# Kernel tuning notes

Measured on AMD Instinct MI355X. Metric: run time of the kernel, lower is better.

The kernel has to match this reference:

```python
import jax, jax.numpy as jnp
import numpy as np
import math

B, L, D = 2, 2048, 1024
H, KV, HD = 16, 4, 64          # num_heads, num_kv_heads, head_dim
GROUPS = H // KV
ROPE_BASE = 10000.0


def _alibi_slopes(n_heads):
    def pow2(n):
        start = 2.0 ** (-(2.0 ** (-(math.log2(n) - 3))))
        return [start * (start ** i) for i in range(n)]
    if math.log2(n_heads).is_integer():
        return pow2(n_heads)
    c = 2 ** math.floor(math.log2(n_heads))
    return pow2(c) + _alibi_slopes(2 * c)[0::2][: n_heads - c]


def _rope_cos_sin(seq_len, dim, dtype):
    inv_freq = 1.0 / (ROPE_BASE ** (jnp.arange(0, dim, 2, dtype=jnp.float32) / dim))
    t = jnp.arange(seq_len, dtype=jnp.float32)
    freqs = t[:, None] * inv_freq[None, :]          # [L, dim/2]
    emb = jnp.concatenate([freqs, freqs], axis=-1)  # [L, dim]
    return jnp.cos(emb).astype(dtype), jnp.sin(emb).astype(dtype)


def _rotate_half(x):
    x1, x2 = x[..., : x.shape[-1] // 2], x[..., x.shape[-1] // 2 :]
    return jnp.concatenate([-x2, x1], axis=-1)


def setup_inputs() -> dict:
    key = jax.random.key(0)
    ks = jax.random.split(key, 5)
    s = 0.02
    return {
        "x": jax.random.normal(ks[0], (B, L, D), jnp.float32),
        "Wq": jax.random.normal(ks[1], (D, H * HD), jnp.float32) * s,
        "Wk": jax.random.normal(ks[2], (D, KV * HD), jnp.float32) * s,
        "Wv": jax.random.normal(ks[3], (D, KV * HD), jnp.float32) * s,
        "Wo": jax.random.normal(ks[4], (H * HD, D), jnp.float32) * s,
    }


def reference(x, Wq, Wk, Wv, Wo):
    b, l, _ = x.shape
    q = (x @ Wq).reshape(b, l, H, HD).transpose(0, 2, 1, 3)   # [B,H,L,hd]
    k = (x @ Wk).reshape(b, l, KV, HD).transpose(0, 2, 1, 3)  # [B,KV,L,hd]
    v = (x @ Wv).reshape(b, l, KV, HD).transpose(0, 2, 1, 3)
    # MQA broadcast: repeat_interleave over head dim
    k = jnp.repeat(k, GROUPS, axis=1)  # [B,H,L,hd]
    v = jnp.repeat(v, GROUPS, axis=1)

    cos, sin = _rope_cos_sin(l, HD, x.dtype)  # [L,hd]
    q = q * cos + _rotate_half(q) * sin
    k = k * cos + _rotate_half(k) * sin

    attn = jnp.einsum("bhqd,bhkd->bhqk", q, k) / math.sqrt(HD)
    # ALiBi bias: (j - i) * slope_h
    pos = jnp.arange(l)
    rel = (pos[None, :] - pos[:, None]).astype(x.dtype)        # [L,L]
    slopes = jnp.asarray(_alibi_slopes(H), dtype=x.dtype)      # [H]
    attn = attn + slopes[None, :, None, None] * rel[None, None, :, :]

    attn = jax.nn.softmax(attn, axis=-1)
    out = jnp.einsum("bhqk,bhkd->bhqd", attn, v)               # [B,H,L,hd]
    out = out.transpose(0, 2, 1, 3).reshape(b, l, H * HD)
    return out @ Wo
```

## Files before the change

kernel.cpp:

```cpp
#include <hip/hip_runtime.h>
#include <math.h>

typedef unsigned short u16;
typedef unsigned int u32;
typedef __attribute__((ext_vector_type(8))) short short8;
typedef __attribute__((ext_vector_type(4))) short short4v;
typedef __attribute__((ext_vector_type(4))) float floatx4;
typedef __attribute__((ext_vector_type(2))) unsigned int uint2v;

#define HN 16
#define KVN 4
#define HDN 64
#define BN_ 2
#define LN 2048
#define DN 1024

__device__ __forceinline__ u16 f2bf(float f) {
    u32 u = __float_as_uint(f);
    u32 r = (u + 0x7fffu + ((u >> 16) & 1u)) >> 16;
    return (u16)r;
}

__device__ __forceinline__ u32 pack2bf(float f0, float f1) {
    u32 u0 = __float_as_uint(f0);
    u32 u1 = __float_as_uint(f1);
    u0 += 0x7fffu + ((u0 >> 16) & 1u);
    u1 += 0x7fffu + ((u1 >> 16) & 1u);
    return __builtin_amdgcn_perm(u1, u0, 0x07060302u);
}

__device__ __forceinline__ void gl16(const u16* g, u16* l) {
    __builtin_amdgcn_global_load_lds(
        (const __attribute__((address_space(1))) u32*)g,
        (__attribute__((address_space(3))) u32*)l, 16, 0, 0);
}

__device__ __forceinline__ void do_transpose(const float* __restrict__ W, u16* __restrict__ WT,
                                             int R, int C, int bx, int by, int tid,
                                             float (*t)[33]) {
    int tx = tid & 31, ty = tid >> 5;
    int c0 = bx * 32, r0 = by * 32;
#pragma unroll
    for (int i = 0; i < 4; i++) {
        int r = r0 + ty + i * 8;
        t[ty + i * 8][tx] = W[(size_t)r * C + c0 + tx];
    }
    __syncthreads();
#pragma unroll
    for (int i = 0; i < 4; i++) {
        int c = c0 + ty + i * 8;
        WT[(size_t)c * R + r0 + tx] = f2bf(t[tx][ty + i * 8]);
    }
}

__global__ __launch_bounds__(256) void prep_kernel(const float* __restrict__ x,
                                                   const float* __restrict__ Wq,
                                                   const float* __restrict__ Wk,
                                                   const float* __restrict__ Wv,
                                                   const float* __restrict__ Wo,
                                                   u16* __restrict__ xb,
                                                   u16* __restrict__ WT,
                                                   u16* __restrict__ WoT) {
    __shared__ float t[32][33];
    int blk = blockIdx.x, tid = threadIdx.x;
    if (blk < 4096) {
        int i = blk * 256 + tid;
        floatx4 v = ((const floatx4*)x)[i];
        short4v o;
        o[0] = (short)f2bf(v[0]);
        o[1] = (short)f2bf(v[1]);
        o[2] = (short)f2bf(v[2]);
        o[3] = (short)f2bf(v[3]);
        ((short4v*)xb)[i] = o;
    } else if (blk < 5120) {
        int z = blk - 4096;
        do_transpose(Wq, WT, 1024, 1024, z & 31, z >> 5, tid, t);
    } else if (blk < 5376) {
        int z = blk - 5120;
        do_transpose(Wk, WT + 1024 * 1024, 1024, 256, z & 7, z >> 3, tid, t);
    } else if (blk < 5632) {
        int z = blk - 5376;
        do_transpose(Wv, WT + 1280 * 1024, 1024, 256, z & 7, z >> 3, tid, t);
    } else {
        int z = blk - 5632;
        do_transpose(Wo, WoT, 1024, 1024, z & 31, z >> 5, tid, t);
    }
}

__global__ __launch_bounds__(256) void gemm_qkv_rope(const u16* __restrict__ A,
                                                     const u16* __restrict__ BT,
                                                     u16* __restrict__ Qb,
                                                     u16* __restrict__ Kb,
                                                     u16* __restrict__ Vt) {
    __shared__ u16 sm[12288];
    const int K = 1024;
    int tid = threadIdx.x;
    int w = tid >> 6, l = tid & 63, quad = l >> 4, l16 = l & 15;
    int wm = w * 32;
    floatx4 acc[2][4];
#pragma unroll
    for (int i = 0; i < 2; i++)
#pragma unroll
        for (int j = 0; j < 4; j++) acc[i][j] = (floatx4){0.f, 0.f, 0.f, 0.f};
    const u16* ag0 = A + (size_t)(blockIdx.y * 128 + (tid >> 2)) * K + (tid & 3) * 8;
    const u16* ag1 = ag0 + (size_t)64 * K;
    const u16* bg = BT + (size_t)(blockIdx.x * 64 + (tid >> 2)) * K + (tid & 3) * 8;
    int lbase = tid * 8;
    gl16(ag0, &sm[lbase]);
    gl16(ag1, &sm[2048 + lbase]);
    gl16(bg, &sm[4096 + lbase]);
    for (int it = 0; it < 32; it++) {
        __syncthreads();
        int cur = it & 1;
        if (it + 1 < 32) {
            int nb = (cur ^ 1) * 6144;
            ag0 += 32; ag1 += 32; bg += 32;
            gl16(ag0, &sm[nb + lbase]);
            gl16(ag1, &sm[nb + 2048 + lbase]);
            gl16(bg, &sm[nb + 4096 + lbase]);
        }
        const u16* sa = &sm[cur * 6144];
        const u16* sb = sa + 4096;
        short8 af[2], bfr[4];
#pragma unroll
        for (int mt = 0; mt < 2; mt++) af[mt] = *(const short8*)&sa[(wm + mt * 16 + l16) * 32 + quad * 8];
#pragma unroll
        for (int nt = 0; nt < 4; nt++) bfr[nt] = *(const short8*)&sb[(nt * 16 + l16) * 32 + quad * 8];
#pragma unroll
        for (int mt = 0; mt < 2; mt++)
#pragma unroll
            for (int nt = 0; nt < 4; nt++)
                acc[mt][nt] = __builtin_amdgcn_mfma_f32_16x16x32_bf16(af[mt], bfr[nt], acc[mt][nt], 0, 0, 0);
    }
    int bx = blockIdx.x;
    int row0 = blockIdx.y * 128 + wm;
    const float L2R32 = 0.4152410118609203f;
    if (bx < 20) {
        int isK = (bx >= 16);
        int head = isK ? (bx - 16) : bx;
        u16* dst = isK ? Kb : Qb;
        size_t bstride = (size_t)(isK ? KVN : HN) * LN * HDN;
        float invf[2];
#pragma unroll
        for (int ntp = 0; ntp < 2; ntp++) invf[ntp] = exp2f(-(float)(ntp * 16 + l16) * L2R32);
        dst += (size_t)head * LN * HDN;
#pragma unroll
        for (int mt = 0; mt < 2; mt++)
#pragma unroll
            for (int r = 0; r < 4; r++) {
                int row = row0 + mt * 16 + quad * 4 + r;
                int b = row >> 11;
                int lpos = row & 2047;
                float lf = (float)lpos;
#pragma unroll
                for (int ntp = 0; ntp < 2; ntp++) {
                    float th = lf * invf[ntp];
                    float s, c;
                    __sincosf(th, &s, &c);
                    float x1 = acc[mt][ntp][r], x2 = acc[mt][ntp + 2][r];
                    size_t base = (size_t)b * bstride + ((size_t)lpos) * HDN + ntp * 16 + l16;
                    dst[base] = f2bf(x1 * c - x2 * s);
                    dst[base + 32] = f2bf(x2 * c + x1 * s);
                }
            }
    } else {
        int kv = bx - 20;
#pragma unroll
        for (int mt = 0; mt < 2; mt++)
#pragma unroll
            for (int r = 0; r < 4; r++) {
                int row = row0 + mt * 16 + quad * 4 + r;
                int b = row >> 11;
                int lpos = row & 2047;
#pragma unroll
                for (int nt = 0; nt < 4; nt++) {
                    int d = nt * 16 + l16;
                    Vt[(((size_t)b * KVN + kv) * HDN + d) * LN + lpos] = f2bf(acc[mt][nt][r]);
                }
            }
    }
}

__global__ __launch_bounds__(256) void gemm_out(const u16* __restrict__ A,
                                                const u16* __restrict__ BT,
                                                float* __restrict__ C) {
    __shared__ u16 sm[12288];
    const int K = 1024, N = 1024;
    int tid = threadIdx.x;
    int w = tid >> 6, l = tid & 63, quad = l >> 4, l16 = l & 15;
    int wm = w * 32;
    floatx4 acc[2][4];
#pragma unroll
    for (int i = 0; i < 2; i++)
#pragma unroll
        for (int j = 0; j < 4; j++) acc[i][j] = (floatx4){0.f, 0.f, 0.f, 0.f};
    const u16* ag0 = A + (size_t)(blockIdx.y * 128 + (tid >> 2)) * K + (tid & 3) * 8;
    const u16* ag1 = ag0 + (size_t)64 * K;
    const u16* bg = BT + (size_t)(blockIdx.x * 64 + (tid >> 2)) * K + (tid & 3) * 8;
    int lbase = tid * 8;
    gl16(ag0, &sm[lbase]);
    gl16(ag1, &sm[2048 + lbase]);
    gl16(bg, &sm[4096 + lbase]);
    for (int it = 0; it < 32; it++) {
        __syncthreads();
        int cur = it & 1;
        if (it + 1 < 32) {
            int nb = (cur ^ 1) * 6144;
            ag0 += 32; ag1 += 32; bg += 32;
            gl16(ag0, &sm[nb + lbase]);
            gl16(ag1, &sm[nb + 2048 + lbase]);
            gl16(bg, &sm[nb + 4096 + lbase]);
        }
        const u16* sa = &sm[cur * 6144];
        const u16* sb = sa + 4096;
        short8 af[2], bfr[4];
#pragma unroll
        for (int mt = 0; mt < 2; mt++) af[mt] = *(const short8*)&sa[(wm + mt * 16 + l16) * 32 + quad * 8];
#pragma unroll
        for (int nt = 0; nt < 4; nt++) bfr[nt] = *(const short8*)&sb[(nt * 16 + l16) * 32 + quad * 8];
#pragma unroll
        for (int mt = 0; mt < 2; mt++)
#pragma unroll
            for (int nt = 0; nt < 4; nt++)
                acc[mt][nt] = __builtin_amdgcn_mfma_f32_16x16x32_bf16(af[mt], bfr[nt], acc[mt][nt], 0, 0, 0);
    }
#pragma unroll
    for (int mt = 0; mt < 2; mt++)
#pragma unroll
        for (int r = 0; r < 4; r++) {
            int row = blockIdx.y * 128 + wm + mt * 16 + quad * 4 + r;
#pragma unroll
            for (int nt = 0; nt < 4; nt++) {
                int col = blockIdx.x * 64 + nt * 16 + l16;
                C[(size_t)row * N + col] = acc[mt][nt][r];
            }
        }
}

static __device__ const signed char hA_tab[8] = {15, 14, 13, 12, 11, 10, 9, 8};
static __device__ const signed char nA_tab[8] = {32, 32, 32, 32, 32, 24, 17, 12};
static __device__ const signed char hB_tab[8] = {0, 1, 2, 3, 4, 5, 6, 7};
static __device__ const signed char nB_tab[8] = {1, 2, 2, 3, 3, 5, 6, 9};

__global__ __launch_bounds__(256) void attention_kernel(const u16* __restrict__ Qb,
                                                        const u16* __restrict__ Kb,
                                                        const u16* __restrict__ Vt,
                                                        u16* __restrict__ AO) {
    __shared__ u16 sm[20992];
    int rank = blockIdx.x >> 6, sub = blockIdx.x & 63;
    int b = sub >> 5, qb = sub & 31;
    int tid = threadIdx.x, w = tid >> 6, l = tid & 63, quad = l >> 4, l16 = l & 15;
    const float LOG2E = 1.4426950408889634f;
    u16* pb = &sm[16384 + w * 1152];
    int lbase = tid * 8;
    short8 ones;
#pragma unroll
    for (int z = 0; z < 8; z++) ones[z] = (short)0x3F80;
#pragma unroll 1
    for (int task = 0; task < 2; task++) {
        int h = task ? hB_tab[rank] : hA_tab[rank];
        int nit = task ? nB_tab[rank] : nA_tab[rank];
        int ks0 = LN - nit * 64;
        int kv = h >> 2;
        const u16* Kbase = Kb + (((size_t)b * KVN + kv) * LN) * HDN;
        const u16* Vbase = Vt + (((size_t)b * KVN + kv) * HDN) * LN;
        const u16* Qrow = Qb + (((size_t)b * HN + h) * LN + qb * 64 + w * 16 + l16) * HDN;
        short8 bq0 = *(const short8*)&Qrow[quad * 8];
        short8 bq1 = *(const short8*)&Qrow[32 + quad * 8];
        float sLE = exp2f(-0.5f * (float)(h + 1)) * LOG2E;
        float c1 = 0.125f * LOG2E;
        float koff[4][4];
#pragma unroll
        for (int nt = 0; nt < 4; nt++)
#pragma unroll
            for (int r = 0; r < 4; r++)
                koff[nt][r] = fmaf(sLE, (float)(ks0 + nt * 16 + quad * 4 + r - (LN - 1)), -17.312340491f);
        float kbrun = 0.0f, kstep = 64.0f * sLE;
        floatx4 O[4], lacc;
        lacc = (floatx4){0.f, 0.f, 0.f, 0.f};
#pragma unroll
        for (int md = 0; md < 4; md++) O[md] = (floatx4){0.f, 0.f, 0.f, 0.f};
        const u16* kg = Kbase + (size_t)(ks0 + 16 * w + (l >> 2)) * 64 + (l & 3) * 8;
        const u16* vg = Vbase + (size_t)(16 * w + (l >> 2)) * 2048 + ks0 + (l & 3) * 8;
        __syncthreads();
        gl16(kg, &sm[lbase]);
        gl16(kg + 32, &sm[2048 + lbase]);
        gl16(vg, &sm[8192 + lbase]);
        gl16(vg + 32, &sm[8192 + 2048 + lbase]);
        for (int it = 0; it < nit; it++) {
            __syncthreads();
            int cur = it & 1;
            if (it + 1 < nit) {
                int nb = (cur ^ 1) * 4096;
                kg += 4096;
                vg += 64;
                gl16(kg, &sm[nb + lbase]);
                gl16(kg + 32, &sm[nb + 2048 + lbase]);
                gl16(vg, &sm[8192 + nb + lbase]);
                gl16(vg + 32, &sm[8192 + nb + 2048 + lbase]);
            }
            const u16* kc = &sm[cur * 4096];
            const u16* vc = &sm[8192 + cur * 4096];
            short8 ak0[4], ak1[4], av0[4], av1[4];
#pragma unroll
            for (int nt = 0; nt < 4; nt++) {
                ak0[nt] = *(const short8*)&kc[(nt * 16 + l16) * 32 + quad * 8];
                ak1[nt] = *(const short8*)&kc[2048 + (nt * 16 + l16) * 32 + quad * 8];
            }
#pragma unroll
            for (int md = 0; md < 4; md++) {
                av0[md] = *(const short8*)&vc[(md * 16 + l16) * 32 + quad * 8];
                av1[md] = *(const short8*)&vc[2048 + (md * 16 + l16) * 32 + quad * 8];
            }
            floatx4 S[4];
#pragma unroll
            for (int nt = 0; nt < 4; nt++) {
                floatx4 sa = (floatx4){0.f, 0.f, 0.f, 0.f};
                sa = __builtin_amdgcn_mfma_f32_16x16x32_bf16(ak0[nt], bq0, sa, 0, 0, 0);
                sa = __builtin_amdgcn_mfma_f32_16x16x32_bf16(ak1[nt], bq1, sa, 0, 0, 0);
                S[nt] = sa;
            }
#pragma unroll
            for (int nt = 0; nt < 4; nt++) {
                float p0 = __builtin_amdgcn_exp2f(S[nt][0] * c1 + (koff[nt][0] + kbrun));
                float p1 = __builtin_amdgcn_exp2f(S[nt][1] * c1 + (koff[nt][1] + kbrun));
                float p2 = __builtin_amdgcn_exp2f(S[nt][2] * c1 + (koff[nt][2] + kbrun));
                float p3 = __builtin_amdgcn_exp2f(S[nt][3] * c1 + (koff[nt][3] + kbrun));
                uint2v pk;
                pk[0] = pack2bf(p0, p1);
                pk[1] = pack2bf(p2, p3);
                *(uint2v*)&pb[l16 * 72 + nt * 16 + quad * 4] = pk;
            }
            kbrun += kstep;
            short8 bp0 = *(const short8*)&pb[l16 * 72 + quad * 8];
            short8 bp1 = *(const short8*)&pb[l16 * 72 + 32 + quad * 8];
#pragma unroll
            for (int md = 0; md < 4; md++) {
                O[md] = __builtin_amdgcn_mfma_f32_16x16x32_bf16(av0[md], bp0, O[md], 0, 0, 0);
                O[md] = __builtin_amdgcn_mfma_f32_16x16x32_bf16(av1[md], bp1, O[md], 0, 0, 0);
            }
            lacc = __builtin_amdgcn_mfma_f32_16x16x32_bf16(ones, bp0, lacc, 0, 0, 0);
            lacc = __builtin_amdgcn_mfma_f32_16x16x32_bf16(ones, bp1, lacc, 0, 0, 0);
        }
        float inv = 1.0f / lacc[0];
        int qg = qb * 64 + w * 16 + l16;
        size_t base = ((size_t)b * LN + qg) * 1024 + h * 64 + quad * 4;
#pragma unroll
        for (int md = 0; md < 4; md++) {
            uint2v pk;
            pk[0] = pack2bf(O[md][0] * inv, O[md][1] * inv);
            pk[1] = pack2bf(O[md][2] * inv, O[md][3] * inv);
            *(uint2v*)&AO[base + md * 16] = pk;
        }
    }
}

extern "C" void kernel_launch(void* const* d_in, const int* in_sizes, int n_in,
                              void* d_out, int out_size, void* d_ws, size_t ws_size,
                              hipStream_t stream) {
    const float* x = (const float*)d_in[0];
    const float* Wq = (const float*)d_in[1];
    const float* Wk = (const float*)d_in[2];
    const float* Wv = (const float*)d_in[3];
    const float* Wo = (const float*)d_in[4];
    float* out = (float*)d_out;
    char* ws = (char*)d_ws;
    u16* xb = (u16*)(ws);
    u16* WT = (u16*)(ws + 8388608);
    u16* WoT = (u16*)(ws + 11534336);
    u16* Qb = (u16*)(ws + 13631488);
    u16* Kb = (u16*)(ws + 22020096);
    u16* Vt = (u16*)(ws + 24117248);
    u16* AO = xb;

    prep_kernel<<<6656, 256, 0, stream>>>(x, Wq, Wk, Wv, Wo, xb, WT, WoT);
    gemm_qkv_rope<<<dim3(24, 32), 256, 0, stream>>>(xb, WT, Qb, Kb, Vt);
    attention_kernel<<<512, 256, 0, stream>>>(Qb, Kb, Vt, AO);
    gemm_out<<<dim3(16, 32), 256, 0, stream>>>(AO, WoT, out);
}
```

Before: 162.8 us.

## Enlarge GEMM tiles to 128x128 with 2x2 warp layout and XCD-aware block mapping

Both the QKV+RoPE GEMM and the output GEMM move from 128x64 to 128x128 block tiles, with each warp computing a 64x64 subtile instead of 32x64. This raises MFMA work per LDS fragment load and halves the block count. Block indices are remapped so that consecutive blocks on the same XCD share A row tiles, which should improve L2 reuse. The cost is higher register pressure (64 accumulators per lane), more LDS per block, and fewer blocks (384 and 256) to fill the CUs.

```diff
diff --git a/kernel.cpp b/kernel.cpp
--- a/kernel.cpp
+++ b/kernel.cpp
@@ -92,60 +92,65 @@
                                                      u16* __restrict__ Qb,
                                                      u16* __restrict__ Kb,
                                                      u16* __restrict__ Vt) {
-    __shared__ u16 sm[12288];
+    __shared__ u16 sm[16384];
     const int K = 1024;
+    int i = blockIdx.x;
+    int xcd = i & 7, j = i >> 3;
+    int by = xcd * 4 + j / 12;
+    int bx = j % 12;
     int tid = threadIdx.x;
     int w = tid >> 6, l = tid & 63, quad = l >> 4, l16 = l & 15;
-    int wm = w * 32;
-    floatx4 acc[2][4];
-#pragma unroll
-    for (int i = 0; i < 2; i++)
-#pragma unroll
-        for (int j = 0; j < 4; j++) acc[i][j] = (floatx4){0.f, 0.f, 0.f, 0.f};
-    const u16* ag0 = A + (size_t)(blockIdx.y * 128 + (tid >> 2)) * K + (tid & 3) * 8;
+    int wm = (w >> 1) * 64, wn = (w & 1) * 64;
+    floatx4 acc[4][4];
+#pragma unroll
+    for (int a = 0; a < 4; a++)
+#pragma unroll
+        for (int c = 0; c < 4; c++) acc[a][c] = (floatx4){0.f, 0.f, 0.f, 0.f};
+    const u16* ag0 = A + (size_t)(by * 128 + (tid >> 2)) * K + (tid & 3) * 8;
     const u16* ag1 = ag0 + (size_t)64 * K;
-    const u16* bg = BT + (size_t)(blockIdx.x * 64 + (tid >> 2)) * K + (tid & 3) * 8;
+    const u16* bg0 = BT + (size_t)(bx * 128 + (tid >> 2)) * K + (tid & 3) * 8;
+    const u16* bg1 = bg0 + (size_t)64 * K;
     int lbase = tid * 8;
     gl16(ag0, &sm[lbase]);
     gl16(ag1, &sm[2048 + lbase]);
-    gl16(bg, &sm[4096 + lbase]);
+    gl16(bg0, &sm[4096 + lbase]);
+    gl16(bg1, &sm[6144 + lbase]);
     for (int it = 0; it < 32; it++) {
         __syncthreads();
         int cur = it & 1;
         if (it + 1 < 32) {
-            int nb = (cur ^ 1) * 6144;
-            ag0 += 32; ag1 += 32; bg += 32;
+            int nb = (cur ^ 1) * 8192;
+            ag0 += 32; ag1 += 32; bg0 += 32; bg1 += 32;
             gl16(ag0, &sm[nb + lbase]);
             gl16(ag1, &sm[nb + 2048 + lbase]);
-            gl16(bg, &sm[nb + 4096 + lbase]);
+            gl16(bg0, &sm[nb + 4096 + lbase]);
+            gl16(bg1, &sm[nb + 6144 + lbase]);
         }
-        const u16* sa = &sm[cur * 6144];
+        const u16* sa = &sm[cur * 8192];
         const u16* sb = sa + 4096;
-        short8 af[2], bfr[4];
-#pragma unroll
-        for (int mt = 0; mt < 2; mt++) af[mt] = *(const short8*)&sa[(wm + mt * 16 + l16) * 32 + quad * 8];
-#pragma unroll
-        for (int nt = 0; nt < 4; nt++) bfr[nt] = *(const short8*)&sb[(nt * 16 + l16) * 32 + quad * 8];
-#pragma unroll
-        for (int mt = 0; mt < 2; mt++)
+        short8 af[4], bfr[4];
+#pragma unroll
+        for (int mt = 0; mt < 4; mt++) af[mt] = *(const short8*)&sa[(wm + mt * 16 + l16) * 32 + quad * 8];
+#pragma unroll
+        for (int nt = 0; nt < 4; nt++) bfr[nt] = *(const short8*)&sb[(wn + nt * 16 + l16) * 32 + quad * 8];
+#pragma unroll
+        for (int mt = 0; mt < 4; mt++)
 #pragma unroll
             for (int nt = 0; nt < 4; nt++)
                 acc[mt][nt] = __builtin_amdgcn_mfma_f32_16x16x32_bf16(af[mt], bfr[nt], acc[mt][nt], 0, 0, 0);
     }
-    int bx = blockIdx.x;
-    int row0 = blockIdx.y * 128 + wm;
+    int row0 = by * 128 + wm;
     const float L2R32 = 0.4152410118609203f;
-    if (bx < 20) {
-        int isK = (bx >= 16);
-        int head = isK ? (bx - 16) : bx;
-        u16* dst = isK ? Kb : Qb;
+    if (bx < 10) {
+        int isK = (bx >= 8);
+        int head = isK ? ((bx - 8) * 2 + (w & 1)) : (bx * 2 + (w & 1));
+        u16* dst = isK ? (Kb + ((size_t)head) * LN * HDN) : (Qb + ((size_t)head) * LN * HDN);
         size_t bstride = (size_t)(isK ? KVN : HN) * LN * HDN;
         float invf[2];
 #pragma unroll
         for (int ntp = 0; ntp < 2; ntp++) invf[ntp] = exp2f(-(float)(ntp * 16 + l16) * L2R32);
-        dst += (size_t)head * LN * HDN;
-#pragma unroll
-        for (int mt = 0; mt < 2; mt++)
+#pragma unroll
+        for (int mt = 0; mt < 4; mt++)
 #pragma unroll
             for (int r = 0; r < 4; r++) {
                 int row = row0 + mt * 16 + quad * 4 + r;
@@ -164,9 +169,9 @@
                 }
             }
     } else {
-        int kv = bx - 20;
-#pragma unroll
-        for (int mt = 0; mt < 2; mt++)
+        int kv = (bx - 10) * 2 + (w & 1);
+#pragma unroll
+        for (int mt = 0; mt < 4; mt++)
 #pragma unroll
             for (int r = 0; r < 4; r++) {
                 int row = row0 + mt * 16 + quad * 4 + r;
@@ -184,57 +189,63 @@
 __global__ __launch_bounds__(256) void gemm_out(const u16* __restrict__ A,
                                                 const u16* __restrict__ BT,
                                                 float* __restrict__ C) {
-    __shared__ u16 sm[12288];
+    __shared__ u16 sm[16384];
     const int K = 1024, N = 1024;
+    int i = blockIdx.x;
+    int xcd = i & 7, j = i >> 3;
+    int by = xcd * 4 + (j >> 3);
+    int bx = j & 7;
     int tid = threadIdx.x;
     int w = tid >> 6, l = tid & 63, quad = l >> 4, l16 = l & 15;
-    int wm = w * 32;
-    floatx4 acc[2][4];
-#pragma unroll
-    for (int i = 0; i < 2; i++)
-#pragma unroll
-        for (int j = 0; j < 4; j++) acc[i][j] = (floatx4){0.f, 0.f, 0.f, 0.f};
-    const u16* ag0 = A + (size_t)(blockIdx.y * 128 + (tid >> 2)) * K + (tid & 3) * 8;
+    int wm = (w >> 1) * 64, wn = (w & 1) * 64;
+    floatx4 acc[4][4];
+#pragma unroll
+    for (int a = 0; a < 4; a++)
+#pragma unroll
+        for (int c = 0; c < 4; c++) acc[a][c] = (floatx4){0.f, 0.f, 0.f, 0.f};
+    const u16* ag0 = A + (size_t)(by * 128 + (tid >> 2)) * K + (tid & 3) * 8;
     const u16* ag1 = ag0 + (size_t)64 * K;
-    const u16* bg = BT + (size_t)(blockIdx.x * 64 + (tid >> 2)) * K + (tid & 3) * 8;
+    const u16* bg0 = BT + (size_t)(bx * 128 + (tid >> 2)) * K + (tid & 3) * 8;
+    const u16* bg1 = bg0 + (size_t)64 * K;
     int lbase = tid * 8;
     gl16(ag0, &sm[lbase]);
     gl16(ag1, &sm[2048 + lbase]);
-    gl16(bg, &sm[4096 + lbase]);
+    gl16(bg0, &sm[4096 + lbase]);
+    gl16(bg1, &sm[6144 + lbase]);
     for (int it = 0; it < 32; it++) {
         __syncthreads();
         int cur = it & 1;
         if (it + 1 < 32) {
-            int nb = (cur ^ 1) * 6144;
-            ag0 += 32; ag1 += 32; bg += 32;
+            int nb = (cur ^ 1) * 8192;
+            ag0 += 32; ag1 += 32; bg0 += 32; bg1 += 32;
             gl16(ag0, &sm[nb + lbase]);
             gl16(ag1, &sm[nb + 2048 + lbase]);
-            gl16(bg, &sm[nb + 4096 + lbase]);
+            gl16(bg0, &sm[nb + 4096 + lbase]);
+            gl16(bg1, &sm[nb + 6144 + lbase]);
         }
-        const u16* sa = &sm[cur * 6144];
+        const u16* sa = &sm[cur * 8192];
         const u16* sb = sa + 4096;
-        short8 af[2], bfr[4];
-#pragma unroll
-        for (int mt = 0; mt < 2; mt++) af[mt] = *(const short8*)&sa[(wm + mt * 16 + l16) * 32 + quad * 8];
-#pragma unroll
-        for (int nt = 0; nt < 4; nt++) bfr[nt] = *(const short8*)&sb[(nt * 16 + l16) * 32 + quad * 8];
-#pragma unroll
-        for (int mt = 0; mt < 2; mt++)
+        short8 af[4], bfr[4];
+#pragma unroll
+        for (int mt = 0; mt < 4; mt++) af[mt] = *(const short8*)&sa[(wm + mt * 16 + l16) * 32 + quad * 8];
+#pragma unroll
+        for (int nt = 0; nt < 4; nt++) bfr[nt] = *(const short8*)&sb[(wn + nt * 16 + l16) * 32 + quad * 8];
+#pragma unroll
+        for (int mt = 0; mt < 4; mt++)
 #pragma unroll
             for (int nt = 0; nt < 4; nt++)
                 acc[mt][nt] = __builtin_amdgcn_mfma_f32_16x16x32_bf16(af[mt], bfr[nt], acc[mt][nt], 0, 0, 0);
     }
 #pragma unroll
-    for (int mt = 0; mt < 2; mt++)
-#pragma unroll
-        for (int r = 0; r < 4; r++) {
-            int row = blockIdx.y * 128 + wm + mt * 16 + quad * 4 + r;
-#pragma unroll
-            for (int nt = 0; nt < 4; nt++) {
-                int col = blockIdx.x * 64 + nt * 16 + l16;
+    for (int mt = 0; mt < 4; mt++)
+#pragma unroll
+        for (int nt = 0; nt < 4; nt++)
+#pragma unroll
+            for (int r = 0; r < 4; r++) {
+                int row = by * 128 + wm + mt * 16 + quad * 4 + r;
+                int col = bx * 128 + wn + nt * 16 + l16;
                 C[(size_t)row * N + col] = acc[mt][nt][r];
             }
-        }
 }
 
 static __device__ const signed char hA_tab[8] = {15, 14, 13, 12, 11, 10, 9, 8};
@@ -374,7 +385,7 @@
     u16* AO = xb;
 
     prep_kernel<<<6656, 256, 0, stream>>>(x, Wq, Wk, Wv, Wo, xb, WT, WoT);
-    gemm_qkv_rope<<<dim3(24, 32), 256, 0, stream>>>(xb, WT, Qb, Kb, Vt);
+    gemm_qkv_rope<<<384, 256, 0, stream>>>(xb, WT, Qb, Kb, Vt);
     attention_kernel<<<512, 256, 0, stream>>>(Qb, Kb, Vt, AO);
-    gemm_out<<<dim3(16, 32), 256, 0, stream>>>(AO, WoT, out);
-}
+    gemm_out<<<256, 256, 0, stream>>>(AO, WoT, out);
+}
```

Result: slower. 166.5 us (+2.3%).
